# Performance work log

Measured on AMD Instinct MI355X. Metric: run time of the kernel, lower is better.

## Reference

```python
import jax, jax.numpy as jnp
import numpy as np

N, E = 50000, 800000
IN_DIM, HID, OUT = 128, 64, 64
NEG_SLOPE = 0.2  # PyG GATConv default leaky_relu slope


def glorot(key, shape):
    fan_in, fan_out = shape[0], shape[-1]
    lim = jnp.sqrt(6.0 / (fan_in + fan_out))
    return jax.random.uniform(key, shape, minval=-lim, maxval=lim, dtype=jnp.float32)


def setup_inputs() -> dict:
    key = jax.random.key(0)
    ks = jax.random.split(key, 10)
    x = jax.random.normal(ks[0], (N, IN_DIM), dtype=jnp.float32)
    edge_index = jax.random.randint(ks[1], (2, E), 0, N, dtype=jnp.int64)
    # GATConv layer 1: heads=2, concat=False
    W1 = glorot(ks[2], (IN_DIM, 2 * HID))
    att_src1 = glorot(ks[3], (1, 2, HID))[0]   # [2, HID]
    att_dst1 = glorot(ks[4], (1, 2, HID))[0]
    b1 = jnp.zeros((HID,), jnp.float32)
    # GATConv layer 2: heads=1, concat=False
    W2 = glorot(ks[5], (HID, OUT))
    att_src2 = glorot(ks[6], (1, 1, OUT))[0]   # [1, OUT]
    att_dst2 = glorot(ks[7], (1, 1, OUT))[0]
    b2 = jnp.zeros((OUT,), jnp.float32)
    return {"x": x, "edge_index": edge_index, "W1": W1, "att_src1": att_src1,
            "att_dst1": att_dst1, "b1": b1, "W2": W2, "att_src2": att_src2,
            "att_dst2": att_dst2, "b2": b2}


def gat_conv(x, src, dst, W, att_src, att_dst, bias, heads, out_ch):
    n = x.shape[0]
    h = (x @ W).reshape(n, heads, out_ch)              # [N,H,C]
    a_src = jnp.einsum('nhc,hc->nh', h, att_src)       # [N,H]
    a_dst = jnp.einsum('nhc,hc->nh', h, att_dst)
    e = jax.nn.leaky_relu(a_src[src] + a_dst[dst], NEG_SLOPE)  # [E,H]
    # softmax over incoming edges per destination node (stable)
    e_max = jax.ops.segment_max(e, dst, num_segments=n)
    ex = jnp.exp(e - e_max[dst])
    denom = jax.ops.segment_sum(ex, dst, num_segments=n)
    alpha = ex / (denom[dst] + 1e-16)                  # [E,H]
    msg = h[src] * alpha[:, :, None]                   # [E,H,C]
    out = jax.ops.segment_sum(msg, dst, num_segments=n)
    return out.mean(axis=1) + bias                     # concat=False -> head mean


def reference(x, edge_index, W1, att_src1, att_dst1, b1, W2, att_src2, att_dst2, b2):
    n = x.shape[0]
    loop = jnp.arange(n, dtype=edge_index.dtype)
    src = jnp.concatenate([edge_index[0], loop])       # PyG add_self_loops
    dst = jnp.concatenate([edge_index[1], loop])
    x1 = gat_conv(x, src, dst, W1, att_src1, att_dst1, b1, 2, HID)
    x1 = jax.nn.elu(x1)
    # eval mode: dropedge and dropout are identity
    out = gat_conv(x1, src, dst, W2, att_src2, att_dst2, b2, 1, OUT)
    return out
```

## Files before the change

kernel.cpp:

```cpp
#include <hip/hip_runtime.h>
#include <math.h>

#define IN_DIM 128
#define HID 64
#define NEG_SLOPE 0.2f
#define CHUNK 4096
#define GCAP 6144
#define SMEM_UNION 53248

typedef __attribute__((ext_vector_type(8))) short bf16x8;
typedef __attribute__((ext_vector_type(4))) float f32x4;
typedef __attribute__((ext_vector_type(2))) float v2f;

__device__ __forceinline__ float wmax(float v){
  #pragma unroll
  for (int o = 32; o > 0; o >>= 1) v = fmaxf(v, __shfl_xor(v, o));
  return v;
}
__device__ __forceinline__ float wsum(float v){
  #pragma unroll
  for (int o = 32; o > 0; o >>= 1) v += __shfl_xor(v, o);
  return v;
}
__device__ __forceinline__ unsigned short f2bf(float f){
  union { float f; unsigned u; } v; v.f = f;
  unsigned r = v.u + 0x7fffu + ((v.u >> 16) & 1u);
  return (unsigned short)(r >> 16);
}
__device__ __forceinline__ float bl(unsigned u){
  union { unsigned u; float f; } v; v.u = u << 16; return v.f;
}
__device__ __forceinline__ float bh(unsigned u){
  union { unsigned u; float f; } v; v.u = u & 0xffff0000u; return v.f;
}
__device__ __forceinline__ v2f up2(unsigned u){
  v2f r; r[0] = bl(u); r[1] = bh(u); return r;
}

__device__ __forceinline__ void incl_scan256(int* sh, int tid){
  #pragma unroll
  for (int off = 1; off < 256; off <<= 1){
    int v = sh[tid];
    if (tid >= off) v += sh[tid - off];
    __syncthreads();
    sh[tid] = v;
    __syncthreads();
  }
}


__device__ void scatter_body(char* smem, const unsigned* __restrict__ packed, int E,
                             const int* __restrict__ binCnt, int* __restrict__ binOff,
                             unsigned* __restrict__ binned, int bx){
  int* ib = (int*)smem;
  int* bc = ib;
  int* lh = ib + 256;
  int* lbase = ib + 512;
  int* gpos = ib + 768;
  int* lcur = ib + 1024;
  unsigned* buf = (unsigned*)(ib + 1280);
  int tid = threadIdx.x;
  int cg = binCnt[tid];
  bc[tid] = cg;
  lh[tid] = 0;
  __syncthreads();
  incl_scan256(bc, tid);
  int binBase_t = bc[tid] - cg;
  int base = bx * CHUNK;
  int rem = E - base;
  unsigned v[CHUNK / 256];
  #pragma unroll
  for (int j = 0; j < CHUNK / 256; j++){
    int i = j * 256 + tid;
    if (i < rem){ v[j] = packed[base + i]; atomicAdd(&lh[v[j] >> 24], 1); }
  }
  __syncthreads();
  lbase[tid] = lh[tid]; __syncthreads();
  incl_scan256(lbase, tid);
  int myExcl = tid ? lbase[tid - 1] : 0;
  __syncthreads();
  lbase[tid] = myExcl;
  lcur[tid] = myExcl;
  if (lh[tid] > 0) gpos[tid] = binBase_t + atomicAdd(&binOff[tid], lh[tid]);
  __syncthreads();
  #pragma unroll
  for (int j = 0; j < CHUNK / 256; j++){
    int i = j * 256 + tid;
    if (i < rem){
      int b = v[j] >> 24;
      int p = atomicAdd(&lcur[b], 1);
      buf[p] = v[j];
    }
  }
  __syncthreads();
  int cn = rem < CHUNK ? rem : CHUNK;
  for (int i = tid; i < cn; i += 256){
    unsigned u = buf[i];
    int b = u >> 24;
    binned[gpos[b] + (i - lbase[b])] = u;
  }
}

__device__ void group_body(char* smem, const unsigned* __restrict__ binned,
                           const int* __restrict__ binCnt, unsigned* __restrict__ sorted,
                           int* __restrict__ row_ptr, int N, int g){
  unsigned* A = (unsigned*)smem;
  unsigned* B = A + GCAP;
  int* ib = (int*)(B + GCAP);
  int* sc = ib;
  int* h2 = ib + 256;
  int* rs = ib + 512;
  int* cur = ib + 768;
  int tid = threadIdx.x;
  int cg = binCnt[tid];
  sc[tid] = cg;
  h2[tid] = 0;
  __syncthreads();
  incl_scan256(sc, tid);
  int base = sc[g] - binCnt[g];
  int cnt = binCnt[g]; if (cnt > GCAP) cnt = GCAP;
  __syncthreads();
  for (int i = tid; i < cnt; i += 256){
    unsigned u = binned[base + i];
    A[i] = u;
    atomicAdd(&h2[(u >> 16) & 255], 1);
  }
  __syncthreads();
  rs[tid] = h2[tid]; __syncthreads();
  incl_scan256(rs, tid);
  int excl = tid ? rs[tid - 1] : 0;
  __syncthreads();
  rs[tid] = excl; cur[tid] = excl;
  int d = g * 256 + tid;
  if (d < N) row_ptr[d] = base + excl;
  __syncthreads();
  for (int i = tid; i < cnt; i += 256){
    unsigned u = A[i];
    int p = atomicAdd(&cur[(u >> 16) & 255], 1);
    B[p] = u;
  }
  __syncthreads();
  for (int i = tid; i < cnt; i += 256)
    sorted[base + i] = B[i];
}


__device__ void gemm1_body(char* smem, const float* __restrict__ X,
                           const unsigned short* __restrict__ Wt,
                           const float* __restrict__ asrc, const float* __restrict__ adst,
                           unsigned short* __restrict__ Hb, float* __restrict__ aa,
                           int n_rows, int n0){
  const int KP = 136, CP = 132;
  unsigned short* xa = (unsigned short*)smem;
  unsigned short* wl = xa + 64 * KP;
  int tid = threadIdx.x;
  for (int idx = tid; idx < 64 * 32; idx += 256){
    int n = idx >> 5, k4 = idx & 31;
    float4 v = make_float4(0.f, 0.f, 0.f, 0.f);
    if (n0 + n < n_rows) v = *(const float4*)&X[(size_t)(n0 + n) * 128 + k4 * 4];
    ushort4 pk; pk.x = f2bf(v.x); pk.y = f2bf(v.y); pk.z = f2bf(v.z); pk.w = f2bf(v.w);
    *(ushort4*)&xa[n * KP + k4 * 4] = pk;
  }
  for (int idx = tid; idx < 128 * 16; idx += 256){
    int n = idx >> 4, k8 = idx & 15;
    uint4 v = *(const uint4*)&Wt[(size_t)n * 128 + k8 * 8];
    *(uint4*)&wl[n * KP + k8 * 8] = v;
  }
  __syncthreads();

  int lane = tid & 63, w = tid >> 6;
  int m = lane & 15, q = lane >> 4;
  f32x4 acc[4][2];
  #pragma unroll
  for (int i = 0; i < 4; i++)
    #pragma unroll
    for (int j = 0; j < 2; j++)
      #pragma unroll
      for (int r = 0; r < 4; r++) acc[i][j][r] = 0.f;
  #pragma unroll
  for (int ks = 0; ks < 4; ks++){
    bf16x8 bg[2];
    #pragma unroll
    for (int j = 0; j < 2; j++)
      bg[j] = *(const bf16x8*)&wl[((2 * w + j) * 16 + m) * KP + ks * 32 + q * 8];
    #pragma unroll
    for (int i = 0; i < 4; i++){
      bf16x8 af = *(const bf16x8*)&xa[(i * 16 + m) * KP + ks * 32 + q * 8];
      #pragma unroll
      for (int j = 0; j < 2; j++)
        acc[i][j] = __builtin_amdgcn_mfma_f32_16x16x32_bf16(af, bg[j], acc[i][j], 0, 0, 0);
    }
  }
  __syncthreads();
  float* C = (float*)smem;
  #pragma unroll
  for (int i = 0; i < 4; i++)
    #pragma unroll
    for (int j = 0; j < 2; j++)
      #pragma unroll
      for (int r = 0; r < 4; r++)
        C[(i * 16 + q * 4 + r) * CP + (2 * w + j) * 16 + m] = acc[i][j][r];
  __syncthreads();

  int row = tid >> 2;
  int c0 = (tid & 3) * 32;
  int n = n0 + row;
  int head = (tid & 3) >> 1;
  float s_p = 0.f, d_p = 0.f;
  unsigned short hb[32];
  #pragma unroll
  for (int c = 0; c < 32; c += 4){
    f32x4 v = *(const f32x4*)&C[row * CP + c0 + c];
    #pragma unroll
    for (int u = 0; u < 4; u++){
      int ch = (c0 + c + u) & 63;
      s_p += v[u] * asrc[head * 64 + ch];
      d_p += v[u] * adst[head * 64 + ch];
      hb[c + u] = f2bf(v[u]);
    }
  }
  if (n < n_rows){
    #pragma unroll
    for (int c = 0; c < 32; c += 8){
      uint4 pk;
      pk.x = (unsigned)hb[c]     | ((unsigned)hb[c + 1] << 16);
      pk.y = (unsigned)hb[c + 2] | ((unsigned)hb[c + 3] << 16);
      pk.z = (unsigned)hb[c + 4] | ((unsigned)hb[c + 5] << 16);
      pk.w = (unsigned)hb[c + 6] | ((unsigned)hb[c + 7] << 16);
      *(uint4*)&Hb[(size_t)n * 128 + c0 + c] = pk;
    }
  }
  s_p += __shfl_xor(s_p, 1);
  d_p += __shfl_xor(d_p, 1);
  if ((tid & 1) == 0 && n < n_rows){
    aa[(size_t)n * 4 + head]     = s_p;
    aa[(size_t)n * 4 + 2 + head] = d_p;
  }
}


__global__ __launch_bounds__(256) void sort_gemm_a(const unsigned* __restrict__ packed, int E,
    const int* __restrict__ binCnt, int* __restrict__ binOff, unsigned* __restrict__ binned,
    int NS, const float* __restrict__ X, const unsigned short* __restrict__ W1t,
    const float* __restrict__ asrc1, const float* __restrict__ adst1,
    unsigned short* __restrict__ h1b, float* __restrict__ aa1, int n_rows){
  __shared__ char smem[SMEM_UNION];
  int bx = blockIdx.x;
  if (bx < NS){
    scatter_body(smem, packed, E, binCnt, binOff, binned, bx);
  } else {
    gemm1_body(smem, X, W1t, asrc1, adst1, h1b, aa1, n_rows, (bx - NS) * 64);
  }
}

__global__ __launch_bounds__(256) void sort_gemm_b(const unsigned* __restrict__ binned,
    const int* __restrict__ binCnt, unsigned* __restrict__ sorted, int* __restrict__ row_ptr,
    int N, int NS, int gofs, const float* __restrict__ X, const unsigned short* __restrict__ W1t,
    const float* __restrict__ asrc1, const float* __restrict__ adst1,
    unsigned short* __restrict__ h1b, float* __restrict__ aa1, int n_rows){
  __shared__ char smem[SMEM_UNION];
  int bx = blockIdx.x;
  if (bx < NS){
    group_body(smem, binned, binCnt, sorted, row_ptr, N, bx);
  } else {
    gemm1_body(smem, X, W1t, asrc1, adst1, h1b, aa1, n_rows, (gofs + bx - NS) * 64);
  }
}


__global__ __launch_bounds__(256) void prep(const int* __restrict__ ei, int E, int NBLK,
                                            unsigned* __restrict__ packed,
                                            int* __restrict__ binCnt,
                                            const float* __restrict__ W1,
                                            const float* __restrict__ W2,
                                            unsigned short* __restrict__ W1t,
                                            unsigned short* __restrict__ W2t,
                                            int* __restrict__ row_ptr, int N){
  int tid = threadIdx.x;
  if ((int)blockIdx.x < NBLK){
    __shared__ int lh[256];
    lh[tid] = 0; __syncthreads();
    int base = blockIdx.x * CHUNK;
    #pragma unroll
    for (int j = 0; j < CHUNK / 256; j++){
      int e = base + j * 256 + tid;
      if (e < E){
        unsigned s = (unsigned)ei[e];
        unsigned d = (unsigned)ei[E + e];
        packed[e] = (d << 16) | s;
        atomicAdd(&lh[d >> 8], 1);
      }
    }
    __syncthreads();
    if (lh[tid] > 0) atomicAdd(&binCnt[tid], lh[tid]);
  } else {
    int t = (blockIdx.x - NBLK) * 256 + tid;
    if (t < 128 * 128){
      int n = t >> 7, k = t & 127;
      W1t[n * 128 + k] = f2bf(W1[k * 128 + n]);
    }
    int t2 = t - 128 * 128;
    if (t2 >= 0 && t2 < 64 * 64){
      int n = t2 >> 6, k = t2 & 63;
      W2t[n * 64 + k] = f2bf(W2[k * 64 + n]);
    }
    if (t == 0) row_ptr[N] = E;
  }
}


__global__ __launch_bounds__(512) void gemm2_mfma(const unsigned short* __restrict__ Xb,
    const unsigned short* __restrict__ Wt, const float* __restrict__ asrc,
    const float* __restrict__ adst, unsigned short* __restrict__ Hb,
    float* __restrict__ aa, int n_rows)
{
  constexpr int K = 64, NC = 64;
  constexpr int MT = 128;
  constexpr int KP = K + 8;
  constexpr int CP = NC + 4;
  constexpr int NFt = NC / 16;
  constexpr int MFW = (MT / 16) / (8 / NFt);
  constexpr unsigned SM1 = (unsigned)(MT + NC) * KP * 2;
  constexpr unsigned SM2 = (unsigned)MT * CP * 4;
  __shared__ char smem[SM1 > SM2 ? SM1 : SM2];
  unsigned short* xa = (unsigned short*)smem;
  unsigned short* wl = xa + MT * KP;
  int tid = threadIdx.x;
  int n0 = blockIdx.x * MT;

  for (int idx = tid; idx < MT * (K / 8); idx += 512){
    int n = idx >> 3, k8 = idx & 7;
    uint4 v = make_uint4(0u, 0u, 0u, 0u);
    if (n0 + n < n_rows) v = *(const uint4*)&Xb[(size_t)(n0 + n) * K + k8 * 8];
    *(uint4*)&xa[n * KP + k8 * 8] = v;
  }
  for (int idx = tid; idx < NC * (K / 8); idx += 512){
    int n = idx >> 3, k8 = idx & 7;
    uint4 v = *(const uint4*)&Wt[(size_t)n * K + k8 * 8];
    *(uint4*)&wl[n * KP + k8 * 8] = v;
  }
  __syncthreads();

  int lane = tid & 63, w = tid >> 6;
  int m = lane & 15, q = lane >> 4;
  int nf = w & 3;
  int mseg = w >> 2;
  f32x4 acc[MFW];
  #pragma unroll
  for (int i = 0; i < MFW; i++)
    #pragma unroll
    for (int r = 0; r < 4; r++) acc[i][r] = 0.f;

  #pragma unroll
  for (int ks = 0; ks < K / 32; ks++){
    bf16x8 bg = *(const bf16x8*)&wl[(nf * 16 + m) * KP + ks * 32 + q * 8];
    #pragma unroll
    for (int i = 0; i < MFW; i++){
      bf16x8 af = *(const bf16x8*)&xa[((mseg * MFW + i) * 16 + m) * KP + ks * 32 + q * 8];
      acc[i] = __builtin_amdgcn_mfma_f32_16x16x32_bf16(af, bg, acc[i], 0, 0, 0);
    }
  }
  __syncthreads();
  float* C = (float*)smem;
  #pragma unroll
  for (int i = 0; i < MFW; i++)
    #pragma unroll
    for (int r = 0; r < 4; r++)
      C[((mseg * MFW + i) * 16 + q * 4 + r) * CP + nf * 16 + m] = acc[i][r];
  __syncthreads();

  constexpr int CH = NC / 4;
  int row = tid >> 2;
  int c0 = (tid & 3) * CH;
  int n = n0 + row;
  float s_p = 0.f, d_p = 0.f;
  unsigned short hb[CH];
  #pragma unroll
  for (int c = 0; c < CH; c += 4){
    f32x4 v = *(const f32x4*)&C[row * CP + c0 + c];
    #pragma unroll
    for (int u = 0; u < 4; u++){
      int ch = (c0 + c + u) & 63;
      s_p += v[u] * asrc[ch];
      d_p += v[u] * adst[ch];
      hb[c + u] = f2bf(v[u]);
    }
  }
  if (n < n_rows){
    #pragma unroll
    for (int c = 0; c < CH; c += 8){
      uint4 pk;
      pk.x = (unsigned)hb[c]     | ((unsigned)hb[c + 1] << 16);
      pk.y = (unsigned)hb[c + 2] | ((unsigned)hb[c + 3] << 16);
      pk.z = (unsigned)hb[c + 4] | ((unsigned)hb[c + 5] << 16);
      pk.w = (unsigned)hb[c + 6] | ((unsigned)hb[c + 7] << 16);
      *(uint4*)&Hb[(size_t)n * NC + c0 + c] = pk;
    }
  }
  s_p += __shfl_xor(s_p, 1);
  d_p += __shfl_xor(d_p, 1);
  s_p += __shfl_xor(s_p, 2);
  d_p += __shfl_xor(d_p, 2);
  if ((tid & 3) == 0 && n < n_rows){
    aa[(size_t)n * 2]     = s_p;
    aa[(size_t)n * 2 + 1] = d_p;
  }
}


__global__ __launch_bounds__(512) void agg_layer1(const int* __restrict__ row_ptr,
                           const unsigned* __restrict__ sorted,
                           const float* __restrict__ aa, const unsigned short* __restrict__ h1b,
                           const float* __restrict__ b1, unsigned short* __restrict__ x1b,
                           int n_nodes){
  int d = (blockIdx.x * blockDim.x + threadIdx.x) >> 6;
  int lane = threadIdx.x & 63;
  if (d >= n_nodes) return;
  int rp0 = row_ptr[d];
  int deg = row_ptr[d + 1] - rp0;
  float2 adv = *(const float2*)&aa[d * 4 + 2];
  int s = -1;
  if (lane < deg) s = (int)(sorted[rp0 + lane] & 0xffffu);
  else if (lane == deg) s = d;
  float e0 = -INFINITY, e1 = -INFINITY;
  if (s >= 0){
    float2 asv = *(const float2*)&aa[s * 4];
    float t0 = asv.x + adv.x;
    float t1 = asv.y + adv.y;
    e0 = t0 >= 0.f ? t0 : NEG_SLOPE * t0;
    e1 = t1 >= 0.f ? t1 : NEG_SLOPE * t1;
  }
  float m0 = wmax(e0), m1 = wmax(e1);
  float p0 = (s >= 0) ? __expf(e0 - m0) : 0.f;
  float p1 = (s >= 0) ? __expf(e1 - m1) : 0.f;
  float al0 = p0 / (wsum(p0) + 1e-16f);
  float al1 = p1 / (wsum(p1) + 1e-16f);
  int ne = deg + 1;
  int g = lane >> 4, c = lane & 15;
  bool hsel = (c < 8);
  const uint4* hp = (const uint4*)h1b;
  v2f acc[4] = {{0.f,0.f},{0.f,0.f},{0.f,0.f},{0.f,0.f}};
  for (int j0 = 0; j0 < ne; j0 += 16){
    uint4 v[4]; float av[4];
    #pragma unroll
    for (int b = 0; b < 4; b++){
      int j = j0 + b * 4 + g;
      int sj = __shfl(s, j);
      float a0 = __shfl(al0, j);
      float a1 = __shfl(al1, j);
      av[b] = hsel ? a0 : a1;
      if (j < ne) v[b] = hp[sj * 16 + c];
    }
    #pragma unroll
    for (int b = 0; b < 4; b++){
      if (j0 + b * 4 + g < ne){
        v2f aw = {av[b], av[b]};
        acc[0] = aw * up2(v[b].x) + acc[0];
        acc[1] = aw * up2(v[b].y) + acc[1];
        acc[2] = aw * up2(v[b].z) + acc[2];
        acc[3] = aw * up2(v[b].w) + acc[3];
      }
    }
  }
  float accf[8] = {acc[0][0], acc[0][1], acc[1][0], acc[1][1],
                   acc[2][0], acc[2][1], acc[3][0], acc[3][1]};
  #pragma unroll
  for (int i = 0; i < 8; i++){
    accf[i] += __shfl_xor(accf[i], 16);
    accf[i] += __shfl_xor(accf[i], 32);
  }
  float outv[8];
  #pragma unroll
  for (int i = 0; i < 8; i++){
    float o = __shfl_xor(accf[i], 8);
    outv[i] = 0.5f * (accf[i] + o);
  }
  if (g == 0 && c < 8){
    unsigned short hb[8];
    #pragma unroll
    for (int i = 0; i < 8; i++){
      float v = outv[i] + b1[c * 8 + i];
      float r = v > 0.f ? v : expm1f(v);
      hb[i] = f2bf(r);
    }
    uint4 pk;
    pk.x = (unsigned)hb[0] | ((unsigned)hb[1] << 16);
    pk.y = (unsigned)hb[2] | ((unsigned)hb[3] << 16);
    pk.z = (unsigned)hb[4] | ((unsigned)hb[5] << 16);
    pk.w = (unsigned)hb[6] | ((unsigned)hb[7] << 16);
    *(uint4*)&x1b[(size_t)d * 64 + c * 8] = pk;
  }
}

__global__ __launch_bounds__(512) void agg_layer2(const int* __restrict__ row_ptr,
                           const unsigned* __restrict__ sorted,
                           const float* __restrict__ aa, const unsigned short* __restrict__ h2b,
                           const float* __restrict__ b2, float* __restrict__ out, int n_nodes){
  int d = (blockIdx.x * blockDim.x + threadIdx.x) >> 6;
  int lane = threadIdx.x & 63;
  if (d >= n_nodes) return;
  int rp0 = row_ptr[d];
  int deg = row_ptr[d + 1] - rp0;
  float ad = aa[d * 2 + 1];
  int s = -1;
  if (lane < deg) s = (int)(sorted[rp0 + lane] & 0xffffu);
  else if (lane == deg) s = d;
  float e = -INFINITY;
  if (s >= 0){
    float t = aa[s * 2 + 0] + ad;
    e = t >= 0.f ? t : NEG_SLOPE * t;
  }
  float m = wmax(e);
  float p = (s >= 0) ? __expf(e - m) : 0.f;
  float al = p / (wsum(p) + 1e-16f);
  int ne = deg + 1;
  int g = lane >> 3, c = lane & 7;
  const uint4* hp = (const uint4*)h2b;
  v2f acc[4] = {{0.f,0.f},{0.f,0.f},{0.f,0.f},{0.f,0.f}};
  for (int j0 = 0; j0 < ne; j0 += 32){
    uint4 v[4]; float av[4];
    #pragma unroll
    for (int b = 0; b < 4; b++){
      int j = j0 + b * 8 + g;
      int sj = __shfl(s, j);
      av[b] = __shfl(al, j);
      if (j < ne) v[b] = hp[sj * 8 + c];
    }
    #pragma unroll
    for (int b = 0; b < 4; b++){
      if (j0 + b * 8 + g < ne){
        v2f aw = {av[b], av[b]};
        acc[0] = aw * up2(v[b].x) + acc[0];
        acc[1] = aw * up2(v[b].y) + acc[1];
        acc[2] = aw * up2(v[b].z) + acc[2];
        acc[3] = aw * up2(v[b].w) + acc[3];
      }
    }
  }
  float accf[8] = {acc[0][0], acc[0][1], acc[1][0], acc[1][1],
                   acc[2][0], acc[2][1], acc[3][0], acc[3][1]};
  #pragma unroll
  for (int i = 0; i < 8; i++){
    accf[i] += __shfl_xor(accf[i], 8);
    accf[i] += __shfl_xor(accf[i], 16);
    accf[i] += __shfl_xor(accf[i], 32);
  }
  if (lane < 8){
    float r[8];
    #pragma unroll
    for (int i = 0; i < 8; i++) r[i] = accf[i] + b2[lane * 8 + i];
    float* q = &out[(size_t)d * 64 + lane * 8];
    *(float4*)q       = make_float4(r[0], r[1], r[2], r[3]);
    *(float4*)(q + 4) = make_float4(r[4], r[5], r[6], r[7]);
  }
}

extern "C" void kernel_launch(void* const* d_in, const int* in_sizes, int n_in,
                              void* d_out, int out_size, void* d_ws, size_t ws_size,
                              hipStream_t stream){
  const float* x     = (const float*)d_in[0];
  const int*   ei    = (const int*)d_in[1];
  const float* W1    = (const float*)d_in[2];
  const float* asrc1 = (const float*)d_in[3];
  const float* adst1 = (const float*)d_in[4];
  const float* b1    = (const float*)d_in[5];
  const float* W2    = (const float*)d_in[6];
  const float* asrc2 = (const float*)d_in[7];
  const float* adst2 = (const float*)d_in[8];
  const float* b2    = (const float*)d_in[9];
  float* out = (float*)d_out;
  int N = in_sizes[0] / IN_DIM;
  int E = in_sizes[1] / 2;
  int NG = (N + 255) >> 8;
  int NBLK = (E + CHUNK - 1) / CHUNK;
  int nagg = (N + 7) / 8;
  int GT = (N + 63) / 64;
  int GA = GT / 2;
  int GB = GT - GA;

  char* p = (char*)d_ws;
  unsigned short* h1b = (unsigned short*)p;  p += (size_t)N * 128 * 2;
  unsigned short* h2b = (unsigned short*)p;  p += (size_t)N * 64 * 2;
  unsigned short* x1b = (unsigned short*)p;  p += (size_t)N * 64 * 2;
  float* aa1 = (float*)p;                    p += (size_t)N * 4 * 4;
  float* aa2 = (float*)p;                    p += (size_t)N * 2 * 4;
  unsigned* packed = (unsigned*)p;           p += (size_t)E * 4;
  unsigned* binned = (unsigned*)p;           p += (size_t)E * 4;
  unsigned* sorted = (unsigned*)p;           p += (size_t)E * 4;
  int* row_ptr   = (int*)p;                  p += (size_t)(N + 1) * 4;
  int* binCnt    = (int*)p;                  p += 256 * 4;
  int* binOff    = (int*)p;                  p += 256 * 4;
  unsigned short* W1t = (unsigned short*)p;  p += 128 * 128 * 2;
  unsigned short* W2t = (unsigned short*)p;

  hipMemsetAsync(binCnt, 0, 512 * sizeof(int), stream);
  prep<<<NBLK + 80, 256, 0, stream>>>(ei, E, NBLK, packed, binCnt,
                                      W1, W2, W1t, W2t, row_ptr, N);
  sort_gemm_a<<<NBLK + GA, 256, 0, stream>>>(packed, E, binCnt, binOff, binned,
                                             NBLK, x, W1t, asrc1, adst1, h1b, aa1, N);
  sort_gemm_b<<<NG + GB, 256, 0, stream>>>(binned, binCnt, sorted, row_ptr, N,
                                           NG, GA, x, W1t, asrc1, adst1, h1b, aa1, N);
  agg_layer1<<<nagg, 512, 0, stream>>>(row_ptr, sorted, aa1, h1b, b1, x1b, N);
  gemm2_mfma<<<(N + 127) / 128, 512, 0, stream>>>(x1b, W2t, asrc2, adst2, h2b, aa2, N);
  agg_layer2<<<nagg, 512, 0, stream>>>(row_ptr, sorted, aa2, h2b, b2, out, N);
}
```

Baseline: 237.4 us.

## Pack two low-degree nodes per wavefront in aggregation, sweep high-degree nodes separately

Both aggregation kernels now give each wavefront two destination nodes, one per 32-lane half, whenever a node has at most 31 in-edges. A few extra blocks scan row_ptr and process the rare nodes with higher in-degree using the original full-wave path. This targets idle lanes, since the mean degree is about 16 and a 64-lane wave per node left most lanes unused. The division is replaced by a hardware reciprocal and expm1f by __expf(v)-1, which trades a little accuracy for fewer instructions.

```diff
diff --git a/kernel.cpp b/kernel.cpp
--- a/kernel.cpp
+++ b/kernel.cpp
@@ -7,6 +7,7 @@
 #define CHUNK 4096
 #define GCAP 6144
 #define SMEM_UNION 53248
+#define NBIGBLK 40
 
 typedef __attribute__((ext_vector_type(8))) short bf16x8;
 typedef __attribute__((ext_vector_type(4))) float f32x4;
@@ -20,6 +21,16 @@
 __device__ __forceinline__ float wsum(float v){
   #pragma unroll
   for (int o = 32; o > 0; o >>= 1) v += __shfl_xor(v, o);
+  return v;
+}
+__device__ __forceinline__ float wmax32(float v){
+  #pragma unroll
+  for (int o = 16; o > 0; o >>= 1) v = fmaxf(v, __shfl_xor(v, o, 32));
+  return v;
+}
+__device__ __forceinline__ float wsum32(float v){
+  #pragma unroll
+  for (int o = 16; o > 0; o >>= 1) v += __shfl_xor(v, o, 32);
   return v;
 }
 __device__ __forceinline__ unsigned short f2bf(float f){
@@ -318,8 +329,7 @@
   constexpr int MT = 128;
   constexpr int KP = K + 8;
   constexpr int CP = NC + 4;
-  constexpr int NFt = NC / 16;
-  constexpr int MFW = (MT / 16) / (8 / NFt);
+  constexpr int MFW = 4;
   constexpr unsigned SM1 = (unsigned)(MT + NC) * KP * 2;
   constexpr unsigned SM2 = (unsigned)MT * CP * 4;
   __shared__ char smem[SM1 > SM2 ? SM1 : SM2];
@@ -408,14 +418,10 @@
 }
 
 
-__global__ __launch_bounds__(512) void agg_layer1(const int* __restrict__ row_ptr,
-                           const unsigned* __restrict__ sorted,
-                           const float* __restrict__ aa, const unsigned short* __restrict__ h1b,
-                           const float* __restrict__ b1, unsigned short* __restrict__ x1b,
-                           int n_nodes){
-  int d = (blockIdx.x * blockDim.x + threadIdx.x) >> 6;
-  int lane = threadIdx.x & 63;
-  if (d >= n_nodes) return;
+__device__ void agg1_one64(int d, int lane, const int* __restrict__ row_ptr,
+                           const unsigned* __restrict__ sorted, const float* __restrict__ aa,
+                           const unsigned short* __restrict__ h1b, const float* __restrict__ b1,
+                           unsigned short* __restrict__ x1b){
   int rp0 = row_ptr[d];
   int deg = row_ptr[d + 1] - rp0;
   float2 adv = *(const float2*)&aa[d * 4 + 2];
@@ -433,8 +439,8 @@
   float m0 = wmax(e0), m1 = wmax(e1);
   float p0 = (s >= 0) ? __expf(e0 - m0) : 0.f;
   float p1 = (s >= 0) ? __expf(e1 - m1) : 0.f;
-  float al0 = p0 / (wsum(p0) + 1e-16f);
-  float al1 = p1 / (wsum(p1) + 1e-16f);
+  float al0 = p0 * __builtin_amdgcn_rcpf(wsum(p0) + 1e-16f);
+  float al1 = p1 * __builtin_amdgcn_rcpf(wsum(p1) + 1e-16f);
   int ne = deg + 1;
   int g = lane >> 4, c = lane & 15;
   bool hsel = (c < 8);
@@ -449,7 +455,7 @@
       float a0 = __shfl(al0, j);
       float a1 = __shfl(al1, j);
       av[b] = hsel ? a0 : a1;
-      if (j < ne) v[b] = hp[sj * 16 + c];
+      if (j < ne) v[b] = hp[(size_t)sj * 16 + c];
     }
     #pragma unroll
     for (int b = 0; b < 4; b++){
@@ -480,7 +486,7 @@
     #pragma unroll
     for (int i = 0; i < 8; i++){
       float v = outv[i] + b1[c * 8 + i];
-      float r = v > 0.f ? v : expm1f(v);
+      float r = v > 0.f ? v : __expf(v) - 1.0f;
       hb[i] = f2bf(r);
     }
     uint4 pk;
@@ -492,13 +498,116 @@
   }
 }
 
-__global__ __launch_bounds__(512) void agg_layer2(const int* __restrict__ row_ptr,
-                           const unsigned* __restrict__ sorted,
-                           const float* __restrict__ aa, const unsigned short* __restrict__ h2b,
-                           const float* __restrict__ b2, float* __restrict__ out, int n_nodes){
-  int d = (blockIdx.x * blockDim.x + threadIdx.x) >> 6;
-  int lane = threadIdx.x & 63;
-  if (d >= n_nodes) return;
+__global__ __launch_bounds__(512) void agg_layer1(const int* __restrict__ row_ptr,
+    const unsigned* __restrict__ sorted, const float* __restrict__ aa,
+    const unsigned short* __restrict__ h1b, const float* __restrict__ b1,
+    unsigned short* __restrict__ x1b, int n_nodes, int npair, int nsweep){
+  int tid = threadIdx.x;
+  int lane = tid & 63;
+  if ((int)blockIdx.x >= npair){
+    int sw = (blockIdx.x - npair) * 8 + (tid >> 6);
+    int chunk = (n_nodes + nsweep - 1) / nsweep;
+    int a = sw * chunk;
+    int bnd = a + chunk; if (bnd > n_nodes) bnd = n_nodes;
+    for (int i0 = a; i0 < bnd; i0 += 64){
+      int idx = i0 + lane;
+      int dg = 0;
+      if (idx < bnd) dg = row_ptr[idx + 1] - row_ptr[idx];
+      unsigned long long m = __ballot(dg > 31);
+      while (m){
+        int bit = __ffsll((long long)m) - 1;
+        m &= m - 1;
+        agg1_one64(i0 + bit, lane, row_ptr, sorted, aa, h1b, b1, x1b);
+      }
+    }
+    return;
+  }
+  int wid = (blockIdx.x << 3) + (tid >> 6);
+  int half = lane >> 5, l32 = lane & 31;
+  int d = wid * 2 + half;
+  if (wid * 2 >= n_nodes) return;
+  bool valid = d < n_nodes;
+  int rp0 = 0, deg = -1;
+  if (valid){ rp0 = row_ptr[d]; deg = row_ptr[d + 1] - rp0; }
+  bool ok = valid && deg <= 31;
+  int ne = ok ? deg + 1 : 0;
+  int s = -1;
+  if (ok){
+    if (l32 < deg) s = (int)(sorted[rp0 + l32] & 0xffffu);
+    else if (l32 == deg) s = d;
+  }
+  float2 adv = make_float2(0.f, 0.f);
+  if (valid) adv = *(const float2*)&aa[d * 4 + 2];
+  float e0 = -INFINITY, e1 = -INFINITY;
+  if (s >= 0){
+    float2 asv = *(const float2*)&aa[s * 4];
+    float t0 = asv.x + adv.x;
+    float t1 = asv.y + adv.y;
+    e0 = t0 >= 0.f ? t0 : NEG_SLOPE * t0;
+    e1 = t1 >= 0.f ? t1 : NEG_SLOPE * t1;
+  }
+  float m0 = wmax32(e0), m1 = wmax32(e1);
+  float p0 = (s >= 0) ? __expf(e0 - m0) : 0.f;
+  float p1 = (s >= 0) ? __expf(e1 - m1) : 0.f;
+  float al0 = p0 * __builtin_amdgcn_rcpf(wsum32(p0) + 1e-16f);
+  float al1 = p1 * __builtin_amdgcn_rcpf(wsum32(p1) + 1e-16f);
+  int g = l32 >> 4, c = l32 & 15;
+  bool hsel = (c < 8);
+  const uint4* hp = (const uint4*)h1b;
+  v2f acc[4] = {{0.f,0.f},{0.f,0.f},{0.f,0.f},{0.f,0.f}};
+  for (int j0 = 0; j0 < ne; j0 += 8){
+    uint4 v[4]; float av[4];
+    #pragma unroll
+    for (int b = 0; b < 4; b++){
+      int j = j0 + b * 2 + g;
+      int sj = __shfl(s, j, 32);
+      float a0 = __shfl(al0, j, 32);
+      float a1 = __shfl(al1, j, 32);
+      av[b] = hsel ? a0 : a1;
+      if (j < ne) v[b] = hp[(size_t)sj * 16 + c];
+    }
+    #pragma unroll
+    for (int b = 0; b < 4; b++){
+      if (j0 + b * 2 + g < ne){
+        v2f aw = {av[b], av[b]};
+        acc[0] = aw * up2(v[b].x) + acc[0];
+        acc[1] = aw * up2(v[b].y) + acc[1];
+        acc[2] = aw * up2(v[b].z) + acc[2];
+        acc[3] = aw * up2(v[b].w) + acc[3];
+      }
+    }
+  }
+  float accf[8] = {acc[0][0], acc[0][1], acc[1][0], acc[1][1],
+                   acc[2][0], acc[2][1], acc[3][0], acc[3][1]};
+  #pragma unroll
+  for (int i = 0; i < 8; i++) accf[i] += __shfl_xor(accf[i], 16, 32);
+  float outv[8];
+  #pragma unroll
+  for (int i = 0; i < 8; i++){
+    float o = __shfl_xor(accf[i], 8, 32);
+    outv[i] = 0.5f * (accf[i] + o);
+  }
+  if (ok && l32 < 8){
+    unsigned short hb[8];
+    #pragma unroll
+    for (int i = 0; i < 8; i++){
+      float v = outv[i] + b1[l32 * 8 + i];
+      float r = v > 0.f ? v : __expf(v) - 1.0f;
+      hb[i] = f2bf(r);
+    }
+    uint4 pk;
+    pk.x = (unsigned)hb[0] | ((unsigned)hb[1] << 16);
+    pk.y = (unsigned)hb[2] | ((unsigned)hb[3] << 16);
+    pk.z = (unsigned)hb[4] | ((unsigned)hb[5] << 16);
+    pk.w = (unsigned)hb[6] | ((unsigned)hb[7] << 16);
+    *(uint4*)&x1b[(size_t)d * 64 + l32 * 8] = pk;
+  }
+}
+
+__device__ void agg2_one64(int d, int lane, const int* __restrict__ row_ptr,
+                           const unsigned* __restrict__ sorted, const float* __restrict__ aa,
+                           const unsigned short* __restrict__ h2b, const float* __restrict__ b2,
+                           float* __restrict__ out){
   int rp0 = row_ptr[d];
   int deg = row_ptr[d + 1] - rp0;
   float ad = aa[d * 2 + 1];
@@ -512,7 +621,7 @@
   }
   float m = wmax(e);
   float p = (s >= 0) ? __expf(e - m) : 0.f;
-  float al = p / (wsum(p) + 1e-16f);
+  float al = p * __builtin_amdgcn_rcpf(wsum(p) + 1e-16f);
   int ne = deg + 1;
   int g = lane >> 3, c = lane & 7;
   const uint4* hp = (const uint4*)h2b;
@@ -524,7 +633,7 @@
       int j = j0 + b * 8 + g;
       int sj = __shfl(s, j);
       av[b] = __shfl(al, j);
-      if (j < ne) v[b] = hp[sj * 8 + c];
+      if (j < ne) v[b] = hp[(size_t)sj * 8 + c];
     }
     #pragma unroll
     for (int b = 0; b < 4; b++){
@@ -550,6 +659,93 @@
     #pragma unroll
     for (int i = 0; i < 8; i++) r[i] = accf[i] + b2[lane * 8 + i];
     float* q = &out[(size_t)d * 64 + lane * 8];
+    *(float4*)q       = make_float4(r[0], r[1], r[2], r[3]);
+    *(float4*)(q + 4) = make_float4(r[4], r[5], r[6], r[7]);
+  }
+}
+
+__global__ __launch_bounds__(512) void agg_layer2(const int* __restrict__ row_ptr,
+    const unsigned* __restrict__ sorted, const float* __restrict__ aa,
+    const unsigned short* __restrict__ h2b, const float* __restrict__ b2,
+    float* __restrict__ out, int n_nodes, int npair, int nsweep){
+  int tid = threadIdx.x;
+  int lane = tid & 63;
+  if ((int)blockIdx.x >= npair){
+    int sw = (blockIdx.x - npair) * 8 + (tid >> 6);
+    int chunk = (n_nodes + nsweep - 1) / nsweep;
+    int a = sw * chunk;
+    int bnd = a + chunk; if (bnd > n_nodes) bnd = n_nodes;
+    for (int i0 = a; i0 < bnd; i0 += 64){
+      int idx = i0 + lane;
+      int dg = 0;
+      if (idx < bnd) dg = row_ptr[idx + 1] - row_ptr[idx];
+      unsigned long long m = __ballot(dg > 31);
+      while (m){
+        int bit = __ffsll((long long)m) - 1;
+        m &= m - 1;
+        agg2_one64(i0 + bit, lane, row_ptr, sorted, aa, h2b, b2, out);
+      }
+    }
+    return;
+  }
+  int wid = (blockIdx.x << 3) + (tid >> 6);
+  int half = lane >> 5, l32 = lane & 31;
+  int d = wid * 2 + half;
+  if (wid * 2 >= n_nodes) return;
+  bool valid = d < n_nodes;
+  int rp0 = 0, deg = -1;
+  if (valid){ rp0 = row_ptr[d]; deg = row_ptr[d + 1] - rp0; }
+  bool ok = valid && deg <= 31;
+  int ne = ok ? deg + 1 : 0;
+  int s = -1;
+  if (ok){
+    if (l32 < deg) s = (int)(sorted[rp0 + l32] & 0xffffu);
+    else if (l32 == deg) s = d;
+  }
+  float ad = valid ? aa[d * 2 + 1] : 0.f;
+  float e = -INFINITY;
+  if (s >= 0){
+    float t = aa[s * 2 + 0] + ad;
+    e = t >= 0.f ? t : NEG_SLOPE * t;
+  }
+  float m = wmax32(e);
+  float p = (s >= 0) ? __expf(e - m) : 0.f;
+  float al = p * __builtin_amdgcn_rcpf(wsum32(p) + 1e-16f);
+  int g = l32 >> 3, c = l32 & 7;
+  const uint4* hp = (const uint4*)h2b;
+  v2f acc[4] = {{0.f,0.f},{0.f,0.f},{0.f,0.f},{0.f,0.f}};
+  for (int j0 = 0; j0 < ne; j0 += 16){
+    uint4 v[4]; float av[4];
+    #pragma unroll
+    for (int b = 0; b < 4; b++){
+      int j = j0 + b * 4 + g;
+      int sj = __shfl(s, j, 32);
+      av[b] = __shfl(al, j, 32);
+      if (j < ne) v[b] = hp[(size_t)sj * 8 + c];
+    }
+    #pragma unroll
+    for (int b = 0; b < 4; b++){
+      if (j0 + b * 4 + g < ne){
+        v2f aw = {av[b], av[b]};
+        acc[0] = aw * up2(v[b].x) + acc[0];
+        acc[1] = aw * up2(v[b].y) + acc[1];
+        acc[2] = aw * up2(v[b].z) + acc[2];
+        acc[3] = aw * up2(v[b].w) + acc[3];
+      }
+    }
+  }
+  float accf[8] = {acc[0][0], acc[0][1], acc[1][0], acc[1][1],
+                   acc[2][0], acc[2][1], acc[3][0], acc[3][1]};
+  #pragma unroll
+  for (int i = 0; i < 8; i++){
+    accf[i] += __shfl_xor(accf[i], 8, 32);
+    accf[i] += __shfl_xor(accf[i], 16, 32);
+  }
+  if (ok && l32 < 8){
+    float r[8];
+    #pragma unroll
+    for (int i = 0; i < 8; i++) r[i] = accf[i] + b2[l32 * 8 + i];
+    float* q = &out[(size_t)d * 64 + l32 * 8];
     *(float4*)q       = make_float4(r[0], r[1], r[2], r[3]);
     *(float4*)(q + 4) = make_float4(r[4], r[5], r[6], r[7]);
   }
@@ -573,7 +769,7 @@
   int E = in_sizes[1] / 2;
   int NG = (N + 255) >> 8;
   int NBLK = (E + CHUNK - 1) / CHUNK;
-  int nagg = (N + 7) / 8;
+  int npair = (N + 15) / 16;
   int GT = (N + 63) / 64;
   int GA = GT / 2;
   int GB = GT - GA;
@@ -600,7 +796,9 @@
                                              NBLK, x, W1t, asrc1, adst1, h1b, aa1, N);
   sort_gemm_b<<<NG + GB, 256, 0, stream>>>(binned, binCnt, sorted, row_ptr, N,
                                            NG, GA, x, W1t, asrc1, adst1, h1b, aa1, N);
-  agg_layer1<<<nagg, 512, 0, stream>>>(row_ptr, sorted, aa1, h1b, b1, x1b, N);
+  agg_layer1<<<npair + NBIGBLK, 512, 0, stream>>>(row_ptr, sorted, aa1, h1b, b1, x1b,
+                                                  N, npair, NBIGBLK * 8);
   gemm2_mfma<<<(N + 127) / 128, 512, 0, stream>>>(x1b, W2t, asrc2, adst2, h2b, aa2, N);
-  agg_layer2<<<nagg, 512, 0, stream>>>(row_ptr, sorted, aa2, h2b, b2, out, N);
-}
+  agg_layer2<<<npair + NBIGBLK, 512, 0, stream>>>(row_ptr, sorted, aa2, h2b, b2, out,
+                                                  N, npair, NBIGBLK * 8);
+}
```

Result: faster. 220.3 us (-7.2%).
